# Kernel tuning notes

Hardware: AMD Instinct MI355X
Metric: run time of the kernel (lower is better)

## Reference

```python
import jax, jax.numpy as jnp
import numpy as np

B, T, I, H = 64, 512, 256, 512


def setup_inputs() -> dict:
    key = jax.random.key(0)
    ks = jax.random.split(key, 5)
    s = 1.0 / np.sqrt(H)  # PyTorch RNN init: U(-1/sqrt(H), 1/sqrt(H))
    x = jax.random.normal(ks[0], (B, T, I), dtype=jnp.float32)
    W_ih0 = jax.random.uniform(ks[1], (H, I), minval=-s, maxval=s, dtype=jnp.float32)
    W_hh0 = jax.random.uniform(ks[2], (H, H), minval=-s, maxval=s, dtype=jnp.float32)
    W_ih1 = jax.random.uniform(ks[3], (H, H), minval=-s, maxval=s, dtype=jnp.float32)
    W_hh1 = jax.random.uniform(ks[4], (H, H), minval=-s, maxval=s, dtype=jnp.float32)
    return {"x": x, "W_ih0": W_ih0, "W_hh0": W_hh0, "W_ih1": W_ih1, "W_hh1": W_hh1}


def _rnn_layer(inp, Wih, Whh):
    # Precompute input projection for all timesteps at once (one big GEMM).
    xw = jnp.einsum('bti,hi->bth', inp, Wih)  # [B, T, H]

    def step(h, xt):
        h = jnp.tanh(xt + h @ Whh.T)
        return h, h

    h0 = jnp.zeros((inp.shape[0], Whh.shape[0]), dtype=inp.dtype)
    _, ys = jax.lax.scan(step, h0, jnp.swapaxes(xw, 0, 1))  # scan over time
    return jnp.swapaxes(ys, 0, 1)  # [B, T, H]


def reference(x, W_ih0, W_hh0, W_ih1, W_hh1):
    # num_layers=2 stacked tanh RNN, bias=False, batch_first, zero initial state
    out = _rnn_layer(x, W_ih0, W_hh0)
    out = _rnn_layer(out, W_ih1, W_hh1)
    return out
```

## Files before the change

### kernel.cpp

```cpp
#include <hip/hip_runtime.h>
#include <math.h>

#define B   64
#define T   512
#define I0  256
#define H   512
#define M   (B*T)

#define NGR 4
#define BGR 16
#define NCH 16
#define CCH 32
#define HS_STRIDE 520

#define RSLOTS 8
#define RING_US ((size_t)RSLOTS * B * H)

typedef __attribute__((ext_vector_type(8))) short short8;
typedef __attribute__((ext_vector_type(4))) float floatx4;

static __device__ __forceinline__ unsigned short f2bf(float f) {
  unsigned u = __float_as_uint(f);
  u += 0x7fff + ((u >> 16) & 1);
  return (unsigned short)(u >> 16);
}

template<int K>
__global__ __launch_bounds__(256)
void gemm_awt(const float* __restrict__ A, const float* __restrict__ W,
              float* __restrict__ C) {
  __shared__ float As[16][68];
  __shared__ float Bs[16][68];
  const int tid = threadIdx.x;
  const int tx = tid & 15, ty = tid >> 4;
  const int m0 = blockIdx.x * 64, n0 = blockIdx.y * 64;
  float acc[4][4] = {};
  for (int k0 = 0; k0 < K; k0 += 16) {
    {
      int e = tid * 4;
      int m = e >> 4, k = e & 15;
      float4 v = *(const float4*)&A[(m0 + m) * K + k0 + k];
      As[k][m] = v.x; As[k+1][m] = v.y; As[k+2][m] = v.z; As[k+3][m] = v.w;
      float4 w = *(const float4*)&W[(n0 + m) * K + k0 + k];
      Bs[k][m] = w.x; Bs[k+1][m] = w.y; Bs[k+2][m] = w.z; Bs[k+3][m] = w.w;
    }
    __syncthreads();
    #pragma unroll
    for (int k = 0; k < 16; ++k) {
      float a[4], w[4];
      *(float4*)a = *(const float4*)&As[k][ty*4];
      *(float4*)w = *(const float4*)&Bs[k][tx*4];
      #pragma unroll
      for (int i = 0; i < 4; ++i)
        #pragma unroll
        for (int j = 0; j < 4; ++j)
          acc[i][j] += a[i] * w[j];
    }
    __syncthreads();
  }
  #pragma unroll
  for (int i = 0; i < 4; ++i) {
    float4 r;
    r.x = acc[i][0]; r.y = acc[i][1]; r.z = acc[i][2]; r.w = acc[i][3];
    *(float4*)&C[(m0 + ty*4 + i) * H + n0 + tx*4] = r;
  }
}

__global__ __launch_bounds__(256)
void pack_w(const float* __restrict__ W, unsigned short* __restrict__ dst) {
  int idx = blockIdx.x * 256 + threadIdx.x;
  int l = idx & 63, i = (idx >> 6) & 15, tau = (idx >> 10) & 1, c = idx >> 11;
  int col = c * CCH + tau * 16 + (l & 15);
  int k0  = i * 32 + (l >> 4) * 8;
  const float* src = &W[col * H + k0];
  unsigned v[4];
  #pragma unroll
  for (int j = 0; j < 4; ++j) {
    unsigned lo = f2bf(src[2*j]);
    unsigned hi = f2bf(src[2*j + 1]);
    v[j] = lo | (hi << 16);
  }
  *(uint4*)&dst[(size_t)idx * 8] = make_uint4(v[0], v[1], v[2], v[3]);
}

__global__ __launch_bounds__(256)
void rnn_fused(const float* __restrict__ xw,
               const unsigned short* __restrict__ wp0,
               const unsigned short* __restrict__ wp1,
               const unsigned short* __restrict__ wp2,
               unsigned short* __restrict__ ring0,
               unsigned short* __restrict__ ring1,
               float* __restrict__ dout)
{
  extern __shared__ unsigned short smem[];
  unsigned short* Ws0 = smem;
  unsigned short* Wi1 = Ws0 + 16384;
  unsigned short* Ws1 = Wi1 + 16384;
  unsigned short* hs0 = Ws1 + 16384;
  unsigned short* hs1 = hs0 + 8320;

  const int tid   = threadIdx.x;
  const int g     = blockIdx.x & 3;
  const int chunk = blockIdx.x >> 2;
  const int c0    = chunk * CCH;
  const int b0    = g * BGR;
  const int wv    = tid >> 6;
  const int lane  = tid & 63;
  const int mrow  = lane & 15;
  const int quad  = lane >> 4;

  {
    const uint4* s0 = (const uint4*)(wp0 + (size_t)chunk * 16384);
    const uint4* s1 = (const uint4*)(wp1 + (size_t)chunk * 16384);
    const uint4* s2 = (const uint4*)(wp2 + (size_t)chunk * 16384);
    uint4* d0 = (uint4*)Ws0; uint4* d1 = (uint4*)Wi1; uint4* d2 = (uint4*)Ws1;
    for (int i = tid; i < 2048; i += 256) { d0[i] = s0[i]; d1[i] = s1[i]; d2[i] = s2[i]; }
  }
  for (int i = tid; i < 2080; i += 256) ((unsigned long long*)hs1)[i] = 0ULL;
  __syncthreads();

  long cnt = 0;

  for (int r = 0; r <= T; ++r) {
    float xv[4];
    if (wv < 2 && r < T) {
      const int ccol = c0 + wv * 16 + mrow;
      #pragma unroll
      for (int i = 0; i < 4; ++i)
        xv[i] = xw[((size_t)(b0 + quad * 4 + i) * T + r) * H + ccol];
    }

    unsigned long long v0[8], v1[8];
    if (r >= 1) {
      const unsigned long long* s0 =
          (const unsigned long long*)(ring0 + (size_t)((r - 1) & (RSLOTS - 1)) * (B * H))
          + b0 * 128;
      const unsigned long long* s1 =
          (const unsigned long long*)(ring1 + (size_t)((r - 2) & (RSLOTS - 1)) * (B * H))
          + b0 * 128;
      const bool need1 = (r >= 2);
      for (;;) {
        #pragma unroll
        for (int j = 0; j < 8; ++j)
          v0[j] = __hip_atomic_load(s0 + j * 256 + tid,
                                    __ATOMIC_RELAXED, __HIP_MEMORY_SCOPE_AGENT);
        if (need1) {
          #pragma unroll
          for (int j = 0; j < 8; ++j)
            v1[j] = __hip_atomic_load(s1 + j * 256 + tid,
                                      __ATOMIC_RELAXED, __HIP_MEMORY_SCOPE_AGENT);
        }
        unsigned long long bad = 0;
        #pragma unroll
        for (int j = 0; j < 8; ++j) {
          unsigned long long w = ~v0[j];
          bad |= (w - 0x0001000100010001ULL) & ~w & 0x8000800080008000ULL;
        }
        if (need1) {
          #pragma unroll
          for (int j = 0; j < 8; ++j) {
            unsigned long long w = ~v1[j];
            bad |= (w - 0x0001000100010001ULL) & ~w & 0x8000800080008000ULL;
          }
        }
        if (bad == 0 || ++cnt > 2000000L) break;
      }
      #pragma unroll
      for (int j = 0; j < 8; ++j) {
        int ii = j * 256 + tid, row = ii >> 7, c8 = ii & 127;
        *(unsigned long long*)&hs0[row * HS_STRIDE + c8 * 4] = v0[j];
      }
      if (need1) {
        #pragma unroll
        for (int j = 0; j < 8; ++j) {
          int ii = j * 256 + tid, row = ii >> 7, c8 = ii & 127;
          *(unsigned long long*)&hs1[row * HS_STRIDE + c8 * 4] = v1[j];
        }
      }
    }
    asm volatile("s_waitcnt lgkmcnt(0)\n\ts_barrier" ::: "memory");
    __builtin_amdgcn_sched_barrier(0);

    if (wv < 2) {
      if (r < T) {
        floatx4 acc = {0.f, 0.f, 0.f, 0.f};
        if (r >= 1) {
          const unsigned short* wb = Ws0 + wv * 8192;
          const unsigned short* ha = hs0 + mrow * HS_STRIDE + quad * 8;
          #pragma unroll
          for (int i = 0; i < 16; ++i) {
            short8 a = *(const short8*)(ha + i * 32);
            short8 b = *(const short8*)(wb + (i * 64 + lane) * 8);
            acc = __builtin_amdgcn_mfma_f32_16x16x32_bf16(a, b, acc, 0, 0, 0);
          }
        }
        const int ccol = c0 + wv * 16 + mrow;
        unsigned short* rdst = ring0 + (size_t)(r & (RSLOTS - 1)) * (B * H);
        unsigned short* rrst = ring0 + (size_t)((r + 4) & (RSLOTS - 1)) * (B * H);
        #pragma unroll
        for (int i = 0; i < 4; ++i) {
          int b = b0 + quad * 4 + i;
          float h = tanhf(acc[i] + xv[i]);
          __hip_atomic_store(rdst + (size_t)b * H + ccol, f2bf(h),
                             __ATOMIC_RELAXED, __HIP_MEMORY_SCOPE_AGENT);
        }
        #pragma unroll
        for (int i = 0; i < 4; ++i) {
          int b = b0 + quad * 4 + i;
          __hip_atomic_store(rrst + (size_t)b * H + ccol, (unsigned short)0xFFFFu,
                             __ATOMIC_RELAXED, __HIP_MEMORY_SCOPE_AGENT);
        }
      }
    } else {
      if (r >= 1) {
        floatx4 acc = {0.f, 0.f, 0.f, 0.f};
        const int tt = wv - 2;
        const unsigned short* wi  = Wi1 + tt * 8192;
        const unsigned short* wh  = Ws1 + tt * 8192;
        const unsigned short* ha0 = hs0 + mrow * HS_STRIDE + quad * 8;
        const unsigned short* ha1 = hs1 + mrow * HS_STRIDE + quad * 8;
        #pragma unroll
        for (int i = 0; i < 16; ++i) {
          short8 a = *(const short8*)(ha0 + i * 32);
          short8 b = *(const short8*)(wi + (i * 64 + lane) * 8);
          acc = __builtin_amdgcn_mfma_f32_16x16x32_bf16(a, b, acc, 0, 0, 0);
        }
        #pragma unroll
        for (int i = 0; i < 16; ++i) {
          short8 a = *(const short8*)(ha1 + i * 32);
          short8 b = *(const short8*)(wh + (i * 64 + lane) * 8);
          acc = __builtin_amdgcn_mfma_f32_16x16x32_bf16(a, b, acc, 0, 0, 0);
        }
        const int ccol = c0 + tt * 16 + mrow;
        const int t2 = r - 1;
        unsigned short* rdst = ring1 + (size_t)(t2 & (RSLOTS - 1)) * (B * H);
        unsigned short* rrst = ring1 + (size_t)((t2 + 4) & (RSLOTS - 1)) * (B * H);
        float hv[4];
        #pragma unroll
        for (int i = 0; i < 4; ++i) {
          int b = b0 + quad * 4 + i;
          float h = tanhf(acc[i]);
          hv[i] = h;
          __hip_atomic_store(rdst + (size_t)b * H + ccol, f2bf(h),
                             __ATOMIC_RELAXED, __HIP_MEMORY_SCOPE_AGENT);
        }
        #pragma unroll
        for (int i = 0; i < 4; ++i) {
          int b = b0 + quad * 4 + i;
          dout[((size_t)b * T + t2) * H + ccol] = hv[i];
          __hip_atomic_store(rrst + (size_t)b * H + ccol, (unsigned short)0xFFFFu,
                             __ATOMIC_RELAXED, __HIP_MEMORY_SCOPE_AGENT);
        }
      }
    }
    asm volatile("s_barrier" ::: "memory");
  }
}

#define SMEM_BYTES ((3 * 16384 + 2 * 8320) * 2)

extern "C" void kernel_launch(void* const* d_in, const int* in_sizes, int n_in,
                              void* d_out, int out_size, void* d_ws, size_t ws_size,
                              hipStream_t stream) {
  const float* x    = (const float*)d_in[0];
  const float* Wih0 = (const float*)d_in[1];
  const float* Whh0 = (const float*)d_in[2];
  const float* Wih1 = (const float*)d_in[3];
  const float* Whh1 = (const float*)d_in[4];
  float* out = (float*)d_out;

  char* ws = (char*)d_ws;
  float* xw = (float*)ws;
  unsigned short* wp0 = (unsigned short*)(ws + (size_t)64*1024*1024);
  unsigned short* wp1 = (unsigned short*)(ws + (size_t)64*1024*1024 + 512*1024);
  unsigned short* wp2 = (unsigned short*)(ws + (size_t)64*1024*1024 + 1024*1024);
  unsigned short* ring0 = (unsigned short*)(ws + (size_t)64*1024*1024 + 1536*1024);
  unsigned short* ring1 = ring0 + RING_US;

  hipMemsetAsync(ring0, 0xFF, 2 * RING_US * sizeof(unsigned short), stream);
  hipFuncSetAttribute((const void*)rnn_fused,
                      hipFuncAttributeMaxDynamicSharedMemorySize, SMEM_BYTES);

  pack_w<<<128, 256, 0, stream>>>(Whh0, wp0);
  pack_w<<<128, 256, 0, stream>>>(Wih1, wp1);
  pack_w<<<128, 256, 0, stream>>>(Whh1, wp2);

  dim3 gg(M/64, H/64);
  gemm_awt<I0><<<gg, 256, 0, stream>>>(x, Wih0, xw);

  rnn_fused<<<NGR * NCH, 256, SMEM_BYTES, stream>>>(
      xw, wp0, wp1, wp2, ring0, ring1, out);
}
```

Before: 1.350 ms.

## Split RNN layers into separate single-wave blocks with register-resident weights and decoupled pipelining

Replaces the 64 four-wave blocks, which ran both layers in lockstep with block barriers and LDS staging, with 128 single-wave blocks. Layer-0 blocks and layer-1 blocks each own 32 output columns for 16 batch rows and keep the recurrent weights in registers. Each block polls the ring directly into MFMA operands, so the LDS copies and block-wide barriers go away, and layer 1 can lag layer 0 by up to 32 steps through a 64-slot ring and a progress-counter throttle. It also swaps tanhf for an exp/rcp approximation, trading some accuracy and register pressure for less time on the serial critical path.

```diff
diff --git a/kernel.cpp b/kernel.cpp
--- a/kernel.cpp
+++ b/kernel.cpp
@@ -7,14 +7,16 @@
 #define H   512
 #define M   (B*T)
 
-#define NGR 4
-#define BGR 16
-#define NCH 16
-#define CCH 32
-#define HS_STRIDE 520
-
-#define RSLOTS 8
-#define RING_US ((size_t)RSLOTS * B * H)
+#define NGR    4
+#define BGR    16
+#define RSLOTS 64
+#define RESET_D 8
+#define SLOT_US (B*H)
+#define RING_US ((size_t)RSLOTS*SLOT_US)
+
+#define NB1 64
+#define NB2 64
+#define POLL_BUDGET 4000000L
 
 typedef __attribute__((ext_vector_type(8))) short short8;
 typedef __attribute__((ext_vector_type(4))) float floatx4;
@@ -23,6 +25,16 @@
   unsigned u = __float_as_uint(f);
   u += 0x7fff + ((u >> 16) & 1);
   return (unsigned short)(u >> 16);
+}
+
+static __device__ __forceinline__ float ftanh(float x) {
+  float e = __expf(2.0f * x);
+  return 1.0f - 2.0f * __builtin_amdgcn_rcpf(e + 1.0f);
+}
+
+static __device__ __forceinline__ unsigned long long sentmask(unsigned long long v) {
+  unsigned long long w = ~v;
+  return (w - 0x0001000100010001ULL) & ~w & 0x8000800080008000ULL;
 }
 
 template<int K>
@@ -70,7 +82,7 @@
 void pack_w(const float* __restrict__ W, unsigned short* __restrict__ dst) {
   int idx = blockIdx.x * 256 + threadIdx.x;
   int l = idx & 63, i = (idx >> 6) & 15, tau = (idx >> 10) & 1, c = idx >> 11;
-  int col = c * CCH + tau * 16 + (l & 15);
+  int col = c * 32 + tau * 16 + (l & 15);
   int k0  = i * 32 + (l >> 4) * 8;
   const float* src = &W[col * H + k0];
   unsigned v[4];
@@ -83,181 +95,210 @@
   *(uint4*)&dst[(size_t)idx * 8] = make_uint4(v[0], v[1], v[2], v[3]);
 }
 
-__global__ __launch_bounds__(256)
+__global__ __launch_bounds__(64)
 void rnn_fused(const float* __restrict__ xw,
                const unsigned short* __restrict__ wp0,
                const unsigned short* __restrict__ wp1,
                const unsigned short* __restrict__ wp2,
                unsigned short* __restrict__ ring0,
                unsigned short* __restrict__ ring1,
-               float* __restrict__ dout)
+               float* __restrict__ dout,
+               int* __restrict__ prog)
 {
-  extern __shared__ unsigned short smem[];
-  unsigned short* Ws0 = smem;
-  unsigned short* Wi1 = Ws0 + 16384;
-  unsigned short* Ws1 = Wi1 + 16384;
-  unsigned short* hs0 = Ws1 + 16384;
-  unsigned short* hs1 = hs0 + 8320;
-
-  const int tid   = threadIdx.x;
-  const int g     = blockIdx.x & 3;
-  const int chunk = blockIdx.x >> 2;
-  const int c0    = chunk * CCH;
-  const int b0    = g * BGR;
-  const int wv    = tid >> 6;
-  const int lane  = tid & 63;
-  const int mrow  = lane & 15;
-  const int quad  = lane >> 4;
-
-  {
-    const uint4* s0 = (const uint4*)(wp0 + (size_t)chunk * 16384);
-    const uint4* s1 = (const uint4*)(wp1 + (size_t)chunk * 16384);
-    const uint4* s2 = (const uint4*)(wp2 + (size_t)chunk * 16384);
-    uint4* d0 = (uint4*)Ws0; uint4* d1 = (uint4*)Wi1; uint4* d2 = (uint4*)Ws1;
-    for (int i = tid; i < 2048; i += 256) { d0[i] = s0[i]; d1[i] = s1[i]; d2[i] = s2[i]; }
+  __shared__ unsigned short wi_lds[16384];
+  const int lane = threadIdx.x;
+  const int mrow = lane & 15, quad = lane >> 4;
+  long cnt = 0;
+
+  if (blockIdx.x < NB1) {
+    const int g  = blockIdx.x & 3;
+    const int wp = blockIdx.x >> 2;
+    const int t0 = wp * 2;
+    const int b0 = g * BGR;
+    short8 w0[16], w1[16];
+    #pragma unroll
+    for (int kt = 0; kt < 16; ++kt) {
+      w0[kt] = *(const short8*)(wp0 + (size_t)(((t0    ) * 16 + kt) * 64 + lane) * 8);
+      w1[kt] = *(const short8*)(wp0 + (size_t)(((t0 + 1) * 16 + kt) * 64 + lane) * 8);
+    }
+    const int ccol0 = t0 * 16 + mrow, ccol1 = ccol0 + 16;
+    int* pg = prog + g * 16;
+
+    for (int r = 0; r < T; ++r) {
+      float xv0[4], xv1[4];
+      #pragma unroll
+      for (int i = 0; i < 4; ++i) {
+        size_t base = ((size_t)(b0 + quad * 4 + i) * T + r) * H;
+        xv0[i] = xw[base + ccol0];
+        xv1[i] = xw[base + ccol1];
+      }
+      floatx4 acc0 = {0.f,0.f,0.f,0.f}, acc1 = {0.f,0.f,0.f,0.f};
+      if (r >= 1) {
+        const unsigned long long* rb = (const unsigned long long*)
+            (ring0 + (size_t)((r - 1) & (RSLOTS - 1)) * SLOT_US
+                   + (size_t)(b0 + mrow) * H);
+        unsigned long long hv[32];
+        for (;;) {
+          #pragma unroll
+          for (int kt = 0; kt < 16; ++kt) {
+            hv[2*kt]   = __hip_atomic_load(rb + kt * 8 + quad * 2,
+                                           __ATOMIC_RELAXED, __HIP_MEMORY_SCOPE_AGENT);
+            hv[2*kt+1] = __hip_atomic_load(rb + kt * 8 + quad * 2 + 1,
+                                           __ATOMIC_RELAXED, __HIP_MEMORY_SCOPE_AGENT);
+          }
+          unsigned long long bad = 0;
+          #pragma unroll
+          for (int j = 0; j < 32; ++j) bad |= sentmask(hv[j]);
+          if (__all(bad == 0) || ++cnt > POLL_BUDGET) break;
+        }
+        #pragma unroll
+        for (int kt = 0; kt < 16; ++kt) {
+          union { unsigned long long u[2]; short8 s; } a;
+          a.u[0] = hv[2*kt]; a.u[1] = hv[2*kt+1];
+          acc0 = __builtin_amdgcn_mfma_f32_16x16x32_bf16(a.s, w0[kt], acc0, 0, 0, 0);
+          acc1 = __builtin_amdgcn_mfma_f32_16x16x32_bf16(a.s, w1[kt], acc1, 0, 0, 0);
+        }
+      }
+      unsigned short* wdst = ring0 + (size_t)(r & (RSLOTS - 1)) * SLOT_US;
+      unsigned short* wrst = ring0 + (size_t)((r + RESET_D) & (RSLOTS - 1)) * SLOT_US;
+      #pragma unroll
+      for (int i = 0; i < 4; ++i) {
+        size_t brow = (size_t)(b0 + quad * 4 + i) * H;
+        __hip_atomic_store(wdst + brow + ccol0, f2bf(ftanh(acc0[i] + xv0[i])),
+                           __ATOMIC_RELAXED, __HIP_MEMORY_SCOPE_AGENT);
+        __hip_atomic_store(wdst + brow + ccol1, f2bf(ftanh(acc1[i] + xv1[i])),
+                           __ATOMIC_RELAXED, __HIP_MEMORY_SCOPE_AGENT);
+      }
+      #pragma unroll
+      for (int i = 0; i < 4; ++i) {
+        size_t brow = (size_t)(b0 + quad * 4 + i) * H;
+        __hip_atomic_store(wrst + brow + ccol0, (unsigned short)0xFFFFu,
+                           __ATOMIC_RELAXED, __HIP_MEMORY_SCOPE_AGENT);
+        __hip_atomic_store(wrst + brow + ccol1, (unsigned short)0xFFFFu,
+                           __ATOMIC_RELAXED, __HIP_MEMORY_SCOPE_AGENT);
+      }
+      if ((r & 7) == 0 && r >= 40) {
+        for (;;) {
+          int mn = 0x7fffffff;
+          #pragma unroll
+          for (int j = 0; j < 16; ++j) {
+            int v = __hip_atomic_load(pg + j, __ATOMIC_RELAXED, __HIP_MEMORY_SCOPE_AGENT);
+            mn = v < mn ? v : mn;
+          }
+          if (r - mn <= 32 || ++cnt > POLL_BUDGET) break;
+          __builtin_amdgcn_s_sleep(8);
+        }
+      }
+    }
+  } else {
+    const int b2 = blockIdx.x - NB1;
+    const int g  = b2 & 3;
+    const int wp = b2 >> 2;
+    const int t0 = wp * 2;
+    const int b0 = g * BGR;
+    {
+      const uint4* s = (const uint4*)(wp1 + (size_t)t0 * 8192);
+      uint4* d = (uint4*)wi_lds;
+      for (int i = lane; i < 2048; i += 64) d[i] = s[i];
+    }
+    short8 wh0[16], wh1[16];
+    #pragma unroll
+    for (int kt = 0; kt < 16; ++kt) {
+      wh0[kt] = *(const short8*)(wp2 + (size_t)(((t0    ) * 16 + kt) * 64 + lane) * 8);
+      wh1[kt] = *(const short8*)(wp2 + (size_t)(((t0 + 1) * 16 + kt) * 64 + lane) * 8);
+    }
+    __syncthreads();
+    const int ccol0 = t0 * 16 + mrow, ccol1 = ccol0 + 16;
+    int* pslot = prog + g * 16 + wp;
+
+    for (int t = 0; t < T; ++t) {
+      const unsigned long long* rb0 = (const unsigned long long*)
+          (ring0 + (size_t)(t & (RSLOTS - 1)) * SLOT_US + (size_t)(b0 + mrow) * H);
+      unsigned long long h1[32];
+      for (;;) {
+        #pragma unroll
+        for (int kt = 0; kt < 16; ++kt) {
+          h1[2*kt]   = __hip_atomic_load(rb0 + kt * 8 + quad * 2,
+                                         __ATOMIC_RELAXED, __HIP_MEMORY_SCOPE_AGENT);
+          h1[2*kt+1] = __hip_atomic_load(rb0 + kt * 8 + quad * 2 + 1,
+                                         __ATOMIC_RELAXED, __HIP_MEMORY_SCOPE_AGENT);
+        }
+        unsigned long long bad = 0;
+        #pragma unroll
+        for (int j = 0; j < 32; ++j) bad |= sentmask(h1[j]);
+        if (__all(bad == 0) || ++cnt > POLL_BUDGET) break;
+      }
+      unsigned long long h2[32];
+      const unsigned long long* rb1 = (const unsigned long long*)
+          (ring1 + (size_t)((t - 1) & (RSLOTS - 1)) * SLOT_US + (size_t)(b0 + mrow) * H);
+      if (t >= 1) {
+        #pragma unroll
+        for (int kt = 0; kt < 16; ++kt) {
+          h2[2*kt]   = __hip_atomic_load(rb1 + kt * 8 + quad * 2,
+                                         __ATOMIC_RELAXED, __HIP_MEMORY_SCOPE_AGENT);
+          h2[2*kt+1] = __hip_atomic_load(rb1 + kt * 8 + quad * 2 + 1,
+                                         __ATOMIC_RELAXED, __HIP_MEMORY_SCOPE_AGENT);
+        }
+      }
+      floatx4 acc0 = {0.f,0.f,0.f,0.f}, acc1 = {0.f,0.f,0.f,0.f};
+      #pragma unroll
+      for (int kt = 0; kt < 16; ++kt) {
+        union { unsigned long long u[2]; short8 s; } a;
+        a.u[0] = h1[2*kt]; a.u[1] = h1[2*kt+1];
+        short8 bi0 = *(const short8*)(wi_lds + (size_t)((kt     ) * 64 + lane) * 8);
+        short8 bi1 = *(const short8*)(wi_lds + (size_t)((16 + kt) * 64 + lane) * 8);
+        acc0 = __builtin_amdgcn_mfma_f32_16x16x32_bf16(a.s, bi0, acc0, 0, 0, 0);
+        acc1 = __builtin_amdgcn_mfma_f32_16x16x32_bf16(a.s, bi1, acc1, 0, 0, 0);
+      }
+      if (t >= 1) {
+        for (;;) {
+          unsigned long long bad = 0;
+          #pragma unroll
+          for (int j = 0; j < 32; ++j) bad |= sentmask(h2[j]);
+          if (__all(bad == 0) || ++cnt > POLL_BUDGET) break;
+          #pragma unroll
+          for (int kt = 0; kt < 16; ++kt) {
+            h2[2*kt]   = __hip_atomic_load(rb1 + kt * 8 + quad * 2,
+                                           __ATOMIC_RELAXED, __HIP_MEMORY_SCOPE_AGENT);
+            h2[2*kt+1] = __hip_atomic_load(rb1 + kt * 8 + quad * 2 + 1,
+                                           __ATOMIC_RELAXED, __HIP_MEMORY_SCOPE_AGENT);
+          }
+        }
+        #pragma unroll
+        for (int kt = 0; kt < 16; ++kt) {
+          union { unsigned long long u[2]; short8 s; } a;
+          a.u[0] = h2[2*kt]; a.u[1] = h2[2*kt+1];
+          acc0 = __builtin_amdgcn_mfma_f32_16x16x32_bf16(a.s, wh0[kt], acc0, 0, 0, 0);
+          acc1 = __builtin_amdgcn_mfma_f32_16x16x32_bf16(a.s, wh1[kt], acc1, 0, 0, 0);
+        }
+      }
+      unsigned short* wdst = ring1 + (size_t)(t & (RSLOTS - 1)) * SLOT_US;
+      unsigned short* wrst = ring1 + (size_t)((t + RESET_D) & (RSLOTS - 1)) * SLOT_US;
+      #pragma unroll
+      for (int i = 0; i < 4; ++i) {
+        int b = b0 + quad * 4 + i;
+        float v0 = ftanh(acc0[i]);
+        float v1 = ftanh(acc1[i]);
+        __hip_atomic_store(wdst + (size_t)b * H + ccol0, f2bf(v0),
+                           __ATOMIC_RELAXED, __HIP_MEMORY_SCOPE_AGENT);
+        __hip_atomic_store(wdst + (size_t)b * H + ccol1, f2bf(v1),
+                           __ATOMIC_RELAXED, __HIP_MEMORY_SCOPE_AGENT);
+        dout[((size_t)b * T + t) * H + ccol0] = v0;
+        dout[((size_t)b * T + t) * H + ccol1] = v1;
+      }
+      #pragma unroll
+      for (int i = 0; i < 4; ++i) {
+        int b = b0 + quad * 4 + i;
+        __hip_atomic_store(wrst + (size_t)b * H + ccol0, (unsigned short)0xFFFFu,
+                           __ATOMIC_RELAXED, __HIP_MEMORY_SCOPE_AGENT);
+        __hip_atomic_store(wrst + (size_t)b * H + ccol1, (unsigned short)0xFFFFu,
+                           __ATOMIC_RELAXED, __HIP_MEMORY_SCOPE_AGENT);
+      }
+      if ((t & 7) == 0 && lane == 0)
+        __hip_atomic_store(pslot, t, __ATOMIC_RELAXED, __HIP_MEMORY_SCOPE_AGENT);
+    }
   }
-  for (int i = tid; i < 2080; i += 256) ((unsigned long long*)hs1)[i] = 0ULL;
-  __syncthreads();
-
-  long cnt = 0;
-
-  for (int r = 0; r <= T; ++r) {
-    float xv[4];
-    if (wv < 2 && r < T) {
-      const int ccol = c0 + wv * 16 + mrow;
-      #pragma unroll
-      for (int i = 0; i < 4; ++i)
-        xv[i] = xw[((size_t)(b0 + quad * 4 + i) * T + r) * H + ccol];
-    }
-
-    unsigned long long v0[8], v1[8];
-    if (r >= 1) {
-      const unsigned long long* s0 =
-          (const unsigned long long*)(ring0 + (size_t)((r - 1) & (RSLOTS - 1)) * (B * H))
-          + b0 * 128;
-      const unsigned long long* s1 =
-          (const unsigned long long*)(ring1 + (size_t)((r - 2) & (RSLOTS - 1)) * (B * H))
-          + b0 * 128;
-      const bool need1 = (r >= 2);
-      for (;;) {
-        #pragma unroll
-        for (int j = 0; j < 8; ++j)
-          v0[j] = __hip_atomic_load(s0 + j * 256 + tid,
-                                    __ATOMIC_RELAXED, __HIP_MEMORY_SCOPE_AGENT);
-        if (need1) {
-          #pragma unroll
-          for (int j = 0; j < 8; ++j)
-            v1[j] = __hip_atomic_load(s1 + j * 256 + tid,
-                                      __ATOMIC_RELAXED, __HIP_MEMORY_SCOPE_AGENT);
-        }
-        unsigned long long bad = 0;
-        #pragma unroll
-        for (int j = 0; j < 8; ++j) {
-          unsigned long long w = ~v0[j];
-          bad |= (w - 0x0001000100010001ULL) & ~w & 0x8000800080008000ULL;
-        }
-        if (need1) {
-          #pragma unroll
-          for (int j = 0; j < 8; ++j) {
-            unsigned long long w = ~v1[j];
-            bad |= (w - 0x0001000100010001ULL) & ~w & 0x8000800080008000ULL;
-          }
-        }
-        if (bad == 0 || ++cnt > 2000000L) break;
-      }
-      #pragma unroll
-      for (int j = 0; j < 8; ++j) {
-        int ii = j * 256 + tid, row = ii >> 7, c8 = ii & 127;
-        *(unsigned long long*)&hs0[row * HS_STRIDE + c8 * 4] = v0[j];
-      }
-      if (need1) {
-        #pragma unroll
-        for (int j = 0; j < 8; ++j) {
-          int ii = j * 256 + tid, row = ii >> 7, c8 = ii & 127;
-          *(unsigned long long*)&hs1[row * HS_STRIDE + c8 * 4] = v1[j];
-        }
-      }
-    }
-    asm volatile("s_waitcnt lgkmcnt(0)\n\ts_barrier" ::: "memory");
-    __builtin_amdgcn_sched_barrier(0);
-
-    if (wv < 2) {
-      if (r < T) {
-        floatx4 acc = {0.f, 0.f, 0.f, 0.f};
-        if (r >= 1) {
-          const unsigned short* wb = Ws0 + wv * 8192;
-          const unsigned short* ha = hs0 + mrow * HS_STRIDE + quad * 8;
-          #pragma unroll
-          for (int i = 0; i < 16; ++i) {
-            short8 a = *(const short8*)(ha + i * 32);
-            short8 b = *(const short8*)(wb + (i * 64 + lane) * 8);
-            acc = __builtin_amdgcn_mfma_f32_16x16x32_bf16(a, b, acc, 0, 0, 0);
-          }
-        }
-        const int ccol = c0 + wv * 16 + mrow;
-        unsigned short* rdst = ring0 + (size_t)(r & (RSLOTS - 1)) * (B * H);
-        unsigned short* rrst = ring0 + (size_t)((r + 4) & (RSLOTS - 1)) * (B * H);
-        #pragma unroll
-        for (int i = 0; i < 4; ++i) {
-          int b = b0 + quad * 4 + i;
-          float h = tanhf(acc[i] + xv[i]);
-          __hip_atomic_store(rdst + (size_t)b * H + ccol, f2bf(h),
-                             __ATOMIC_RELAXED, __HIP_MEMORY_SCOPE_AGENT);
-        }
-        #pragma unroll
-        for (int i = 0; i < 4; ++i) {
-          int b = b0 + quad * 4 + i;
-          __hip_atomic_store(rrst + (size_t)b * H + ccol, (unsigned short)0xFFFFu,
-                             __ATOMIC_RELAXED, __HIP_MEMORY_SCOPE_AGENT);
-        }
-      }
-    } else {
-      if (r >= 1) {
-        floatx4 acc = {0.f, 0.f, 0.f, 0.f};
-        const int tt = wv - 2;
-        const unsigned short* wi  = Wi1 + tt * 8192;
-        const unsigned short* wh  = Ws1 + tt * 8192;
-        const unsigned short* ha0 = hs0 + mrow * HS_STRIDE + quad * 8;
-        const unsigned short* ha1 = hs1 + mrow * HS_STRIDE + quad * 8;
-        #pragma unroll
-        for (int i = 0; i < 16; ++i) {
-          short8 a = *(const short8*)(ha0 + i * 32);
-          short8 b = *(const short8*)(wi + (i * 64 + lane) * 8);
-          acc = __builtin_amdgcn_mfma_f32_16x16x32_bf16(a, b, acc, 0, 0, 0);
-        }
-        #pragma unroll
-        for (int i = 0; i < 16; ++i) {
-          short8 a = *(const short8*)(ha1 + i * 32);
-          short8 b = *(const short8*)(wh + (i * 64 + lane) * 8);
-          acc = __builtin_amdgcn_mfma_f32_16x16x32_bf16(a, b, acc, 0, 0, 0);
-        }
-        const int ccol = c0 + tt * 16 + mrow;
-        const int t2 = r - 1;
-        unsigned short* rdst = ring1 + (size_t)(t2 & (RSLOTS - 1)) * (B * H);
-        unsigned short* rrst = ring1 + (size_t)((t2 + 4) & (RSLOTS - 1)) * (B * H);
-        float hv[4];
-        #pragma unroll
-        for (int i = 0; i < 4; ++i) {
-          int b = b0 + quad * 4 + i;
-          float h = tanhf(acc[i]);
-          hv[i] = h;
-          __hip_atomic_store(rdst + (size_t)b * H + ccol, f2bf(h),
-                             __ATOMIC_RELAXED, __HIP_MEMORY_SCOPE_AGENT);
-        }
-        #pragma unroll
-        for (int i = 0; i < 4; ++i) {
-          int b = b0 + quad * 4 + i;
-          dout[((size_t)b * T + t2) * H + ccol] = hv[i];
-          __hip_atomic_store(rrst + (size_t)b * H + ccol, (unsigned short)0xFFFFu,
-                             __ATOMIC_RELAXED, __HIP_MEMORY_SCOPE_AGENT);
-        }
-      }
-    }
-    asm volatile("s_barrier" ::: "memory");
-  }
-}
-
-#define SMEM_BYTES ((3 * 16384 + 2 * 8320) * 2)
+}
 
 extern "C" void kernel_launch(void* const* d_in, const int* in_sizes, int n_in,
                               void* d_out, int out_size, void* d_ws, size_t ws_size,
@@ -276,10 +317,10 @@
   unsigned short* wp2 = (unsigned short*)(ws + (size_t)64*1024*1024 + 1024*1024);
   unsigned short* ring0 = (unsigned short*)(ws + (size_t)64*1024*1024 + 1536*1024);
   unsigned short* ring1 = ring0 + RING_US;
+  int* prog = (int*)(ring1 + RING_US);
 
   hipMemsetAsync(ring0, 0xFF, 2 * RING_US * sizeof(unsigned short), stream);
-  hipFuncSetAttribute((const void*)rnn_fused,
-                      hipFuncAttributeMaxDynamicSharedMemorySize, SMEM_BYTES);
+  hipMemsetAsync(prog, 0, NGR * 16 * sizeof(int), stream);
 
   pack_w<<<128, 256, 0, stream>>>(Whh0, wp0);
   pack_w<<<128, 256, 0, stream>>>(Wih1, wp1);
@@ -288,6 +329,6 @@
   dim3 gg(M/64, H/64);
   gemm_awt<I0><<<gg, 256, 0, stream>>>(x, Wih0, xw);
 
-  rnn_fused<<<NGR * NCH, 256, SMEM_BYTES, stream>>>(
-      xw, wp0, wp1, wp2, ring0, ring1, out);
-}
+  rnn_fused<<<NB1 + NB2, 64, 0, stream>>>(
+      xw, wp0, wp1, wp2, ring0, ring1, out, prog);
+}
```

Measured after the change: 1.985 ms. 47.1% more time.

## Replace FP32 input-projection GEMM with split-bf16 MFMA and use fast tanh

Applied to the files above, without the earlier changes.

The scalar FP32 SIMT GEMM that computed the layer-0 input projection is replaced by an MFMA bf16 kernel. It splits x into high and low bf16 parts and uses weights packed into MFMA fragment order, staged in 128 KB of shared memory. The projection result is now stored as bf16, which halves both the workspace and the per-step reads in the recurrent kernel. tanhf is replaced with an exp plus reciprocal approximation. Together these add rounding error: bf16 weights and output in the projection, plus the approximate tanh.

```diff
diff --git a/kernel.cpp b/kernel.cpp
--- a/kernel.cpp
+++ b/kernel.cpp
@@ -24,46 +24,12 @@
   u += 0x7fff + ((u >> 16) & 1);
   return (unsigned short)(u >> 16);
 }
-
-template<int K>
-__global__ __launch_bounds__(256)
-void gemm_awt(const float* __restrict__ A, const float* __restrict__ W,
-              float* __restrict__ C) {
-  __shared__ float As[16][68];
-  __shared__ float Bs[16][68];
-  const int tid = threadIdx.x;
-  const int tx = tid & 15, ty = tid >> 4;
-  const int m0 = blockIdx.x * 64, n0 = blockIdx.y * 64;
-  float acc[4][4] = {};
-  for (int k0 = 0; k0 < K; k0 += 16) {
-    {
-      int e = tid * 4;
-      int m = e >> 4, k = e & 15;
-      float4 v = *(const float4*)&A[(m0 + m) * K + k0 + k];
-      As[k][m] = v.x; As[k+1][m] = v.y; As[k+2][m] = v.z; As[k+3][m] = v.w;
-      float4 w = *(const float4*)&W[(n0 + m) * K + k0 + k];
-      Bs[k][m] = w.x; Bs[k+1][m] = w.y; Bs[k+2][m] = w.z; Bs[k+3][m] = w.w;
-    }
-    __syncthreads();
-    #pragma unroll
-    for (int k = 0; k < 16; ++k) {
-      float a[4], w[4];
-      *(float4*)a = *(const float4*)&As[k][ty*4];
-      *(float4*)w = *(const float4*)&Bs[k][tx*4];
-      #pragma unroll
-      for (int i = 0; i < 4; ++i)
-        #pragma unroll
-        for (int j = 0; j < 4; ++j)
-          acc[i][j] += a[i] * w[j];
-    }
-    __syncthreads();
-  }
-  #pragma unroll
-  for (int i = 0; i < 4; ++i) {
-    float4 r;
-    r.x = acc[i][0]; r.y = acc[i][1]; r.z = acc[i][2]; r.w = acc[i][3];
-    *(float4*)&C[(m0 + ty*4 + i) * H + n0 + tx*4] = r;
-  }
+static __device__ __forceinline__ float bf2f(unsigned short u) {
+  return __uint_as_float((unsigned)u << 16);
+}
+static __device__ __forceinline__ float ftanh(float x) {
+  float e = __expf(2.0f * x);
+  return 1.0f - 2.0f * __builtin_amdgcn_rcpf(e + 1.0f);
 }
 
 __global__ __launch_bounds__(256)
@@ -84,7 +50,69 @@
 }
 
 __global__ __launch_bounds__(256)
-void rnn_fused(const float* __restrict__ xw,
+void pack_wx(const float* __restrict__ W, unsigned short* __restrict__ dst) {
+  int idx = blockIdx.x * 256 + threadIdx.x;
+  int l = idx & 63, kt = (idx >> 6) & 7, t = idx >> 9;
+  int col = t * 16 + (l & 15);
+  int k0  = kt * 32 + (l >> 4) * 8;
+  const float* src = &W[col * I0 + k0];
+  unsigned v[4];
+  #pragma unroll
+  for (int j = 0; j < 4; ++j) {
+    unsigned lo = f2bf(src[2*j]);
+    unsigned hi = f2bf(src[2*j + 1]);
+    v[j] = lo | (hi << 16);
+  }
+  *(uint4*)&dst[(size_t)idx * 8] = make_uint4(v[0], v[1], v[2], v[3]);
+}
+
+__global__ __launch_bounds__(256)
+void gemm_mfma(const float* __restrict__ x, const unsigned short* __restrict__ wpx,
+               unsigned short* __restrict__ xwb) {
+  extern __shared__ unsigned short wl[];
+  const int tid = threadIdx.x, wv = tid >> 6, lane = tid & 63;
+  const int mrow = lane & 15, quad = lane >> 4;
+  const int m0 = blockIdx.x * 64 + wv * 16;
+  const int n0 = blockIdx.y * 256;
+  {
+    const uint4* s = (const uint4*)(wpx + (size_t)(n0 / 16) * 4096);
+    uint4* d = (uint4*)wl;
+    for (int i = tid; i < 8192; i += 256) d[i] = s[i];
+  }
+  short8 ah[8], al[8];
+  const float* xr = x + (size_t)(m0 + mrow) * I0;
+  #pragma unroll
+  for (int kt = 0; kt < 8; ++kt) {
+    float4 u = *(const float4*)&xr[kt * 32 + quad * 8];
+    float4 v = *(const float4*)&xr[kt * 32 + quad * 8 + 4];
+    float f[8] = {u.x,u.y,u.z,u.w,v.x,v.y,v.z,v.w};
+    union { unsigned w[4]; short8 s; } hi, lo;
+    #pragma unroll
+    for (int j = 0; j < 4; ++j) {
+      unsigned short h0 = f2bf(f[2*j]),   l0 = f2bf(f[2*j]   - bf2f(h0));
+      unsigned short h1 = f2bf(f[2*j+1]), l1 = f2bf(f[2*j+1] - bf2f(h1));
+      hi.w[j] = (unsigned)h0 | ((unsigned)h1 << 16);
+      lo.w[j] = (unsigned)l0 | ((unsigned)l1 << 16);
+    }
+    ah[kt] = hi.s; al[kt] = lo.s;
+  }
+  __syncthreads();
+  for (int ct = 0; ct < 16; ++ct) {
+    floatx4 acc = {0.f,0.f,0.f,0.f};
+    #pragma unroll
+    for (int kt = 0; kt < 8; ++kt) {
+      short8 b = *(const short8*)(wl + ((size_t)(ct * 8 + kt) * 64 + lane) * 8);
+      acc = __builtin_amdgcn_mfma_f32_16x16x32_bf16(al[kt], b, acc, 0, 0, 0);
+      acc = __builtin_amdgcn_mfma_f32_16x16x32_bf16(ah[kt], b, acc, 0, 0, 0);
+    }
+    #pragma unroll
+    for (int i = 0; i < 4; ++i)
+      xwb[(size_t)(m0 + quad*4 + i) * H + n0 + ct*16 + mrow] = f2bf(acc[i]);
+  }
+}
+
+__global__ __launch_bounds__(256)
+void rnn_fused(const unsigned short* __restrict__ xwb,
                const unsigned short* __restrict__ wp0,
                const unsigned short* __restrict__ wp1,
                const unsigned short* __restrict__ wp2,
@@ -122,12 +150,12 @@
   long cnt = 0;
 
   for (int r = 0; r <= T; ++r) {
-    float xv[4];
+    unsigned short xus[4];
     if (wv < 2 && r < T) {
       const int ccol = c0 + wv * 16 + mrow;
       #pragma unroll
       for (int i = 0; i < 4; ++i)
-        xv[i] = xw[((size_t)(b0 + quad * 4 + i) * T + r) * H + ccol];
+        xus[i] = xwb[((size_t)(b0 + quad * 4 + i) * T + r) * H + ccol];
     }
 
     unsigned long long v0[8], v1[8];
@@ -200,7 +228,7 @@
         #pragma unroll
         for (int i = 0; i < 4; ++i) {
           int b = b0 + quad * 4 + i;
-          float h = tanhf(acc[i] + xv[i]);
+          float h = ftanh(acc[i] + bf2f(xus[i]));
           __hip_atomic_store(rdst + (size_t)b * H + ccol, f2bf(h),
                              __ATOMIC_RELAXED, __HIP_MEMORY_SCOPE_AGENT);
         }
@@ -239,7 +267,7 @@
         #pragma unroll
         for (int i = 0; i < 4; ++i) {
           int b = b0 + quad * 4 + i;
-          float h = tanhf(acc[i]);
+          float h = ftanh(acc[i]);
           hv[i] = h;
           __hip_atomic_store(rdst + (size_t)b * H + ccol, f2bf(h),
                              __ATOMIC_RELAXED, __HIP_MEMORY_SCOPE_AGENT);
@@ -258,6 +286,7 @@
 }
 
 #define SMEM_BYTES ((3 * 16384 + 2 * 8320) * 2)
+#define SMEM_GEMM  131072
 
 extern "C" void kernel_launch(void* const* d_in, const int* in_sizes, int n_in,
                               void* d_out, int out_size, void* d_ws, size_t ws_size,
@@ -270,24 +299,28 @@
   float* out = (float*)d_out;
 
   char* ws = (char*)d_ws;
-  float* xw = (float*)ws;
-  unsigned short* wp0 = (unsigned short*)(ws + (size_t)64*1024*1024);
-  unsigned short* wp1 = (unsigned short*)(ws + (size_t)64*1024*1024 + 512*1024);
-  unsigned short* wp2 = (unsigned short*)(ws + (size_t)64*1024*1024 + 1024*1024);
-  unsigned short* ring0 = (unsigned short*)(ws + (size_t)64*1024*1024 + 1536*1024);
+  unsigned short* xwb = (unsigned short*)ws;
+  unsigned short* wp0 = (unsigned short*)(ws + (size_t)32*1024*1024);
+  unsigned short* wp1 = (unsigned short*)(ws + (size_t)32*1024*1024 + 512*1024);
+  unsigned short* wp2 = (unsigned short*)(ws + (size_t)32*1024*1024 + 1024*1024);
+  unsigned short* wpx = (unsigned short*)(ws + (size_t)32*1024*1024 + 1536*1024);
+  unsigned short* ring0 = (unsigned short*)(ws + (size_t)32*1024*1024 + 1792*1024);
   unsigned short* ring1 = ring0 + RING_US;
 
   hipMemsetAsync(ring0, 0xFF, 2 * RING_US * sizeof(unsigned short), stream);
   hipFuncSetAttribute((const void*)rnn_fused,
                       hipFuncAttributeMaxDynamicSharedMemorySize, SMEM_BYTES);
+  hipFuncSetAttribute((const void*)gemm_mfma,
+                      hipFuncAttributeMaxDynamicSharedMemorySize, SMEM_GEMM);
 
   pack_w<<<128, 256, 0, stream>>>(Whh0, wp0);
   pack_w<<<128, 256, 0, stream>>>(Wih1, wp1);
   pack_w<<<128, 256, 0, stream>>>(Whh1, wp2);
-
-  dim3 gg(M/64, H/64);
-  gemm_awt<I0><<<gg, 256, 0, stream>>>(x, Wih0, xw);
+  pack_wx<<<64, 256, 0, stream>>>(Wih0, wpx);
+
+  dim3 gg(M/64, H/256);
+  gemm_mfma<<<gg, 256, SMEM_GEMM, stream>>>(x, wpx, xwb);
 
   rnn_fused<<<NGR * NCH, 256, SMEM_BYTES, stream>>>(
-      xw, wp0, wp1, wp2, ring0, ring1, out);
-}
+      xwb, wp0, wp1, wp2, ring0, ring1, out);
+}
```

Result: faster. 1.217 ms (-9.8%).
